# Optimization experiments

Measured on AMD Instinct MI355X. Metric: run time of the kernel, lower is better.

The kernel has to match this reference:

```python
import jax, jax.numpy as jnp
import numpy as np

B, N, D = 64, 1024, 512
H, LD = 8, 64            # num_heads, linear_hidden_dim (H*LD == D)
HIDDEN = 4 * D           # ffn_multiply = 4.0
NB = 128                 # number of timestamp buckets
EPS = 1e-6
TS_SCALE = NB / 14.0     # log1p(1e6) ~ 13.8 -> buckets span [0, NB]


def rms_norm(x, eps=EPS):
    return x * jax.lax.rsqrt(jnp.mean(x * x, axis=-1, keepdims=True) + eps)


def setup_inputs() -> dict:
    key = jax.random.key(0)
    ks = jax.random.split(key, 8)
    lengths = np.linspace(256, N, B).astype(np.int64)
    x_offsets = jnp.asarray(np.concatenate([[0], np.cumsum(lengths)]), dtype=jnp.int64)
    T = int(lengths.sum())
    x = jax.random.normal(ks[0], (T, D), dtype=jnp.float32)
    all_timestamps = jnp.sort(jax.random.randint(ks[1], (B, N), 0, 10**6, dtype=jnp.int64), axis=1)
    invalid_attn_mask = jnp.tril(jnp.ones((N, N), jnp.float32))  # causal
    uv = jax.random.normal(ks[2], (D, 3 * H * LD), dtype=jnp.float32) * 0.02
    pos_w = jax.random.normal(ks[3], (2 * N - 1,), dtype=jnp.float32) * 0.02
    ts_w = jax.random.normal(ks[4], (NB + 1,), dtype=jnp.float32) * 0.02
    w_ams = jax.random.normal(ks[5], (2 * H * LD, D), dtype=jnp.float32) * 0.02
    w1 = jax.random.normal(ks[6], (D, HIDDEN), dtype=jnp.float32) * 0.02
    w2 = jax.random.normal(ks[7], (HIDDEN, D), dtype=jnp.float32) * 0.02
    return {"x": x, "x_offsets": x_offsets, "all_timestamps": all_timestamps,
            "invalid_attn_mask": invalid_attn_mask, "uv": uv, "pos_w": pos_w,
            "ts_w": ts_w, "w_ams": w_ams, "w1": w1, "w2": w2}


def reference(x, x_offsets, all_timestamps, invalid_attn_mask, uv, pos_w, ts_w, w_ams, w1, w2):
    T = x.shape[0]
    # RMSNorm (no learned scale, matches F.rms_norm with no weight) + fused proj + SiLU
    proj = jax.nn.silu(rms_norm(x) @ uv)                       # [T, 3*H*LD]
    u, v = proj[:, :2 * H * LD], proj[:, 2 * H * LD:]          # [T,2HD'], [T,HD']
    # jagged -> padded dense
    tok = jnp.arange(T)
    seg = jnp.searchsorted(x_offsets, tok, side="right") - 1   # batch id per token
    pos = tok - x_offsets[seg]                                  # position within sequence
    padded_v = jnp.zeros((B, N, H * LD), v.dtype).at[seg, pos].set(v).reshape(B, N, H, LD)
    # positional relative bias (batch-independent)
    rel = jnp.arange(N)[:, None] - jnp.arange(N)[None, :]
    pos_attn = pos_w[rel + N - 1] * invalid_attn_mask           # [N,N]
    # temporal relative bias: log-bucketized |t_i - t_j|
    dt = jnp.abs(all_timestamps[:, :, None] - all_timestamps[:, None, :]).astype(jnp.float32)
    bucket = jnp.clip(jnp.floor(jnp.log1p(dt) * TS_SCALE), 0, NB).astype(jnp.int32)
    ts_attn = ts_w[bucket] * invalid_attn_mask[None]            # [B,N,N]
    # two-stream bias 'attention' (no softmax)
    out_pos = jnp.einsum("nm,bmhd->bnhd", pos_attn, padded_v)
    out_ts = jnp.einsum("bnm,bmhd->bnhd", ts_attn, padded_v)
    combined = jnp.concatenate([out_pos, out_ts], axis=-1).reshape(B, N, 2 * H * LD)
    attn_out = combined[seg, pos]                               # dense -> jagged, [T, 2*H*LD]
    # gated norm + multistage FFN with residuals
    ams = u * rms_norm(attn_out)
    h = x + ams @ w_ams
    out = h + jax.nn.silu(rms_norm(h) @ w1) @ w2
    return out
```

## Files before the change

kernel.cpp:

```cpp
#include <hip/hip_runtime.h>
#include <cmath>


using u16 = unsigned short;
using u8  = unsigned char;

typedef __bf16 bf16x8 __attribute__((ext_vector_type(8)));
typedef __bf16 bf16x2 __attribute__((ext_vector_type(2)));
typedef float  f32x4  __attribute__((ext_vector_type(4)));
typedef float  f32x2  __attribute__((ext_vector_type(2)));

#define TS_SCALE_F (float)(128.0 / 14.0)

__device__ __forceinline__ u16 f2b(float f) {
  unsigned u = __float_as_uint(f);
  unsigned r = 0x7FFFu + ((u >> 16) & 1u);
  return (u16)((u + r) >> 16);
}
__device__ __forceinline__ u16 f2b_n(float f) {
  union { __bf16 b; u16 u; } c; c.b = (__bf16)f; return c.u;
}
__device__ __forceinline__ unsigned cvt_pk2(float a, float b) {
  f32x2 v; v[0] = a; v[1] = b;
  bf16x2 r = __builtin_convertvector(v, bf16x2);
  union { bf16x2 b; unsigned u; } c; c.b = r; return c.u;
}
__device__ __forceinline__ float b2f(u16 v) {
  return __uint_as_float(((unsigned)v) << 16);
}
__device__ __forceinline__ bf16x8 as_frag(uint4 r) {
  union { uint4 u; bf16x8 v; } c; c.u = r; return c.v;
}

__device__ __forceinline__ void gload_lds16(const u16* g, u16* l) {
  __builtin_amdgcn_global_load_lds(
      (const __attribute__((address_space(1))) unsigned int*)g,
      (__attribute__((address_space(3))) unsigned int*)l, 16, 0, 0);
}

__device__ __forceinline__ size_t ts_base_u8(int b, int nt) {
  return (size_t)b * 589824 + (size_t)(nt * (nt + 1) / 2) * 16384;
}

__global__ __launch_bounds__(256) void wprep(
    const float* __restrict__ W, u16* __restrict__ Wp, int K, int N)
{
  const int p = blockIdx.x, s = blockIdx.y;
  const int t = threadIdx.x;
  size_t base = ((size_t)p * (K >> 5) + s) * 4096;
  const int e0 = t * 16;
  u16 o[16];
#pragma unroll
  for (int i = 0; i < 16; ++i) {
    int e = e0 + i;
    int kb = e >> 10, r = e & 1023, c = r >> 3, ke = r & 7;
    o[i] = f2b(W[(size_t)(s * 32 + kb * 8 + ke) * N + p * 128 + c]);
  }
  *(uint4*)(Wp + base + e0)     = *(uint4*)o;
  *(uint4*)(Wp + base + e0 + 8) = *(uint4*)(o + 8);
}

#define EPI_SILU_BF16  0
#define EPI_ADD_F32    1
#define EPI_SILU_IMG   2
#define EPI_ADDS       3
#define AM_BF16   0
#define AM_IMG    3
#define AM_BF16M  5

template <int EPI, int AMODE>
__global__ __launch_bounds__(256, 2) void gemm_bf16(
    const u16* __restrict__ A,
    const float* __restrict__ inv, const u16* __restrict__ U, int ustride,
    const u16* __restrict__ Wp, void* __restrict__ C,
    const float* __restrict__ ADD,
    int M, int N, int K, int ncb)
{
  constexpr int NB_ = (AMODE == AM_IMG) ? 2 : 1;
  constexpr int ASZ = (AMODE == AM_IMG) ? 4096 : 5120;
  __shared__ u16 lA[NB_ * ASZ];
  __shared__ u16 lB[NB_ * 4096];

  const int nblk = gridDim.x;
  const int q = nblk >> 3, r = nblk & 7;
  const int xcd = blockIdx.x & 7, li = blockIdx.x >> 3;
  const int work = xcd * q + (xcd < r ? xcd : r) + li;
  const int c0b = work % ncb;
  const int t0  = (work / ncb) * 128;
  const int c0  = c0b * 128;

  const int tid  = threadIdx.x;
  const int wave = tid >> 6, lane = tid & 63;
  const int wr   = (wave >> 1) * 64, wc = (wave & 1) * 64;
  const int l15  = lane & 15, l4 = lane >> 4;

  f32x4 z = {0.f, 0.f, 0.f, 0.f};
  f32x4 acc[4][4];
#pragma unroll
  for (int m = 0; m < 4; ++m)
#pragma unroll
    for (int j = 0; j < 4; ++j) acc[m][j] = z;

  const int ksteps = K >> 5;
  const u16* wsrc = Wp + (size_t)c0b * ksteps * 4096 + wave * 1024 + lane * 8;

  if constexpr (AMODE == AM_IMG) {
    const u16* asrc = A + (size_t)(t0 >> 7) * ksteps * 4096 + wave * 1024 + lane * 8;
    auto stage = [&](int b) {
      u16* sb = &lB[b * 4096 + wave * 1024];
      u16* sa = &lA[b * 4096 + wave * 1024];
      gload_lds16(wsrc,       sb);
      gload_lds16(wsrc + 512, sb + 512);
      gload_lds16(asrc,       sa);
      gload_lds16(asrc + 512, sa + 512);
      wsrc += 4096; asrc += 4096;
    };
    auto compute = [&](int b) {
      bf16x8 afr[4], bfv[4];
#pragma unroll
      for (int m = 0; m < 4; ++m)
        afr[m] = as_frag(*(const uint4*)&lA[b * 4096 + (l4 << 10) + (wr + m * 16 + l15) * 8]);
#pragma unroll
      for (int j = 0; j < 4; ++j)
        bfv[j] = as_frag(*(const uint4*)&lB[b * 4096 + (l4 << 10) + (wc + j * 16 + l15) * 8]);
#pragma unroll
      for (int m = 0; m < 4; ++m)
#pragma unroll
        for (int j = 0; j < 4; ++j)
          acc[m][j] = __builtin_amdgcn_mfma_f32_16x16x32_bf16(afr[m], bfv[j], acc[m][j], 0, 0, 0);
    };
    stage(0);
    int buf = 0;
    for (int s = 0; s + 1 < ksteps; ++s) {
      stage(buf ^ 1);
      asm volatile("s_waitcnt vmcnt(4)" ::: "memory");
      __builtin_amdgcn_s_barrier();
      compute(buf);
      __builtin_amdgcn_s_barrier();
      buf ^= 1;
    }
    asm volatile("s_waitcnt vmcnt(0)" ::: "memory");
    __builtin_amdgcn_s_barrier();
    compute(buf);
  } else {
    const int ar = tid >> 1, ak = (tid & 1) * 16;
    const int row = t0 + ar;
    const bool arow_ok = row < M;
    const u16* ab = A + (size_t)row * K + ak;
    const u16* um = (AMODE == AM_BF16M) ? U + (size_t)row * ustride + ak : nullptr;
    u16* ldsb = &lB[wave * 1024];

    for (int s = 0; s < ksteps; ++s) {
      gload_lds16(wsrc,       ldsb);
      gload_lds16(wsrc + 512, ldsb + 512);
      wsrc += 4096;
      const int k0 = s * 32;
      uint4 pr[4];
      const uint4 z4 = make_uint4(0, 0, 0, 0);
      if (!arow_ok) { pr[0] = z4; pr[1] = z4; pr[2] = z4; pr[3] = z4; }
      else if constexpr (AMODE == AM_BF16) {
        pr[0] = *(const uint4*)(ab + k0);
        pr[1] = *(const uint4*)(ab + k0 + 8);
      } else {
        pr[0] = *(const uint4*)(ab + k0);
        pr[1] = *(const uint4*)(ab + k0 + 8);
        pr[2] = *(const uint4*)(um + k0);
        pr[3] = *(const uint4*)(um + k0 + 8);
      }
      u16 tmp[16];
      unsigned* t32 = (unsigned*)tmp;
      if constexpr (AMODE == AM_BF16) {
        *(uint4*)tmp       = pr[0];
        *(uint4*)(tmp + 8) = pr[1];
      } else {
        const u16* a = (const u16*)pr;
        const u16* u = (const u16*)(pr + 2);
#pragma unroll
        for (int i = 0; i < 8; ++i)
          t32[i] = cvt_pk2(b2f(a[2 * i]) * b2f(u[2 * i]),
                           b2f(a[2 * i + 1]) * b2f(u[2 * i + 1]));
      }
      *(uint4*)&lA[ar * 40 + ak]     = *(uint4*)tmp;
      *(uint4*)&lA[ar * 40 + ak + 8] = *(uint4*)(tmp + 8);
      __syncthreads();

      bf16x8 afr[4], bfv[4];
#pragma unroll
      for (int m = 0; m < 4; ++m)
        afr[m] = as_frag(*(const uint4*)&lA[(wr + m * 16 + l15) * 40 + l4 * 8]);
#pragma unroll
      for (int j = 0; j < 4; ++j)
        bfv[j] = as_frag(*(const uint4*)&lB[(l4 << 10) + (wc + j * 16 + l15) * 8]);
#pragma unroll
      for (int m = 0; m < 4; ++m)
#pragma unroll
        for (int j = 0; j < 4; ++j)
          acc[m][j] = __builtin_amdgcn_mfma_f32_16x16x32_bf16(afr[m], bfv[j], acc[m][j], 0, 0, 0);
      __syncthreads();
    }
  }

#pragma unroll
  for (int m = 0; m < 4; ++m) {
#pragma unroll
    for (int rr = 0; rr < 4; ++rr) {
      int orow = t0 + wr + m * 16 + l4 * 4 + rr;
      if (orow >= M) continue;
      float einv = 0.f;
      if (EPI == EPI_ADDS) einv = inv[orow];
#pragma unroll
      for (int j = 0; j < 4; ++j) {
        int col = c0 + wc + j * 16 + l15;
        float y = acc[m][j][rr];
        if constexpr (EPI == EPI_SILU_BF16) {
          float s = y / (1.f + __expf(-y));
          ((u16*)C)[(size_t)orow * N + col] = f2b_n(s);
        } else if constexpr (EPI == EPI_ADD_F32) {
          size_t idx = (size_t)orow * N + col;
          ((float*)C)[idx] = y + ADD[idx];
        } else if constexpr (EPI == EPI_ADDS) {
          size_t idx = (size_t)orow * N + col;
          ((float*)C)[idx] = y * einv + ADD[idx];
        } else {
          float s = y / (1.f + __expf(-y));
          size_t ioff = ((size_t)(t0 >> 7) * (N >> 5) + (col >> 5)) * 4096
                      + (size_t)((col >> 3) & 3) * 1024
                      + (size_t)(orow & 127) * 8 + (col & 7);
          ((u16*)C)[ioff] = f2b_n(s);
        }
      }
    }
  }
}

__global__ __launch_bounds__(128) void pos_scores(
    const float* __restrict__ pos_w, u16* __restrict__ pos_s)
{
  const int n = blockIdx.x;
  const int m0 = threadIdx.x * 8;
  u16 o[8];
#pragma unroll
  for (int i = 0; i < 8; ++i) {
    int m = m0 + i;
    float v = (m <= n) ? pos_w[n - m + 1023] : 0.f;
    o[i] = f2b(v);
  }
  *(uint4*)(pos_s + (size_t)n * 1024 + m0) = *(uint4*)o;
}

__global__ __launch_bounds__(256) void ts_buckets(
    const int* __restrict__ tstamp, u8* __restrict__ ts_s)
{
  const int nt = 7 - (blockIdx.x >> 6);
  const int b  = blockIdx.x & 63;
  const int W  = 128 * (nt + 1);
  const int n0 = nt * 128;
  const int tid = threadIdx.x;

  __shared__ int tsm[1024];
  for (int i = tid; i < W; i += 256) tsm[i] = tstamp[b * 1024 + i];
  __syncthreads();

  const int r = tid >> 1, h = tid & 1;
  const int n_abs = n0 + r;
  const int t_n = tstamp[b * 1024 + n_abs];
  const int half = W >> 1;
  const int c0 = h * half;
  u8* row = ts_s + ts_base_u8(b, nt) + (size_t)r * W + c0;

  for (int c = 0; c < half; c += 16) {
    u8 o[16];
#pragma unroll
    for (int i = 0; i < 16; ++i) {
      int m = c0 + c + i;
      int d = t_n - tsm[m];
      if (d < 0) d = -d;
      int bkt = (int)(log1pf((float)d) * TS_SCALE_F);
      bkt = bkt > 128 ? 128 : bkt;
      o[i] = (m <= n_abs) ? (u8)bkt : (u8)129;
    }
    *(uint4*)(row + c) = *(uint4*)o;
  }
}

__global__ __launch_bounds__(256, 1) void attn_gemm(
    const u16* __restrict__ proj,
    const int* __restrict__ xoff,
    const u16* __restrict__ pos_s,
    const u8*  __restrict__ tsU8,
    const float* __restrict__ ts_w,
    u16* __restrict__ attn_out,
    int Ttot)
{
  const int flat = blockIdx.x;
  const int nt = 7 - (flat >> 8);
  const int rem = flat & 255;
  const int b  = rem >> 2;
  const int ct = rem & 3;

  const int off = xoff[b];
  int len = xoff[b + 1] - off;
  if (len < 0) len = 0;
  if (len > 1024) len = 1024;
  if (off < 0 || off + len > Ttot) return;
  const int n0 = nt * 128;
  if (n0 >= len) return;
  const int c0 = ct * 128;
  const int W = 128 * (nt + 1);

  __shared__ u16 lP[128 * 40];
  __shared__ u16 lT[128 * 40];
  __shared__ u16 sV[4096];
  __shared__ float s_tsw[130];

  const int tid = threadIdx.x;
  if (tid < 130) s_tsw[tid] = (tid < 129) ? ts_w[tid] : 0.f;
  __syncthreads();

  const int wave = tid >> 6, lane = tid & 63;
  const int wr = (wave >> 1) * 64, wc = (wave & 1) * 64;
  const int l15 = lane & 15, l4 = lane >> 4;

  f32x4 z = {0.f, 0.f, 0.f, 0.f};
  f32x4 accP[4][4], accT[4][4];
#pragma unroll
  for (int m = 0; m < 4; ++m)
#pragma unroll
    for (int j = 0; j < 4; ++j) { accP[m][j] = z; accT[m][j] = z; }

  const int ar = tid >> 1, ak = (tid & 1) * 16;
  const u16* pRow = pos_s + (size_t)(n0 + ar) * 1024 + ak;
  const u8*  tRow = tsU8 + ts_base_u8(b, nt) + (size_t)ar * W + ak;
  const int vk = tid >> 3, vc = (tid & 7) * 16;

  const int mEnd = (n0 + 128 < len) ? (n0 + 128) : len;

  for (int m0 = 0; m0 < mEnd; m0 += 32) {
    {
      int mm = m0 + vk;
      uint4 v0 = make_uint4(0, 0, 0, 0), v1 = v0;
      if (mm < len) {
        const u16* src = proj + (size_t)(off + mm) * 1536 + 1024 + c0 + vc;
        v0 = *(const uint4*)src;
        v1 = *(const uint4*)(src + 8);
      }
      u16 tmp[16];
      *(uint4*)tmp       = v0;
      *(uint4*)(tmp + 8) = v1;
      const int kb = vk >> 3, ke = vk & 7;
#pragma unroll
      for (int i = 0; i < 16; ++i) {
        int col = vc + i;
        int o2 = (kb * 2048 + col * 16 + ke * 2) ^ (((col >> 3) & 7) << 4);
        *(u16*)((char*)sV + o2) = tmp[i];
      }
    }
    {
      uint4 p0 = *(const uint4*)(pRow + m0);
      uint4 p1 = *(const uint4*)(pRow + m0 + 8);
      uint4 tb = *(const uint4*)(tRow + m0);
      const u8* bp = (const u8*)&tb;
      unsigned tt32[8];
#pragma unroll
      for (int i = 0; i < 8; ++i)
        tt32[i] = cvt_pk2(s_tsw[bp[2 * i]], s_tsw[bp[2 * i + 1]]);
      int wb = ar * 40 + ak;
      *(uint4*)&lP[wb]     = p0;
      *(uint4*)&lP[wb + 8] = p1;
      *(uint4*)&lT[wb]     = *(uint4*)tt32;
      *(uint4*)&lT[wb + 8] = *(uint4*)(tt32 + 4);
    }
    __syncthreads();

    bf16x8 ap[4], at[4], bv[4];
#pragma unroll
    for (int m = 0; m < 4; ++m) {
      ap[m] = as_frag(*(const uint4*)&lP[(wr + m * 16 + l15) * 40 + l4 * 8]);
      at[m] = as_frag(*(const uint4*)&lT[(wr + m * 16 + l15) * 40 + l4 * 8]);
    }
#pragma unroll
    for (int j = 0; j < 4; ++j) {
      int col = wc + j * 16 + l15;
      int o2 = (l4 * 2048 + col * 16) ^ (((col >> 3) & 7) << 4);
      bv[j] = as_frag(*(const uint4*)((char*)sV + o2));
    }
#pragma unroll
    for (int m = 0; m < 4; ++m)
#pragma unroll
      for (int j = 0; j < 4; ++j) {
        accP[m][j] = __builtin_amdgcn_mfma_f32_16x16x32_bf16(ap[m], bv[j], accP[m][j], 0, 0, 0);
        accT[m][j] = __builtin_amdgcn_mfma_f32_16x16x32_bf16(at[m], bv[j], accT[m][j], 0, 0, 0);
      }
    __syncthreads();
  }

#pragma unroll
  for (int m = 0; m < 4; ++m)
#pragma unroll
    for (int r = 0; r < 4; ++r) {
      int n = n0 + wr + m * 16 + l4 * 4 + r;
      if (n >= len) continue;
      size_t t = (size_t)(off + n);
#pragma unroll
      for (int j = 0; j < 4; ++j) {
        int hd = c0 + wc + j * 16 + l15;
        int colP = ((hd >> 6) << 7) + (hd & 63);
        attn_out[t * 1024 + colP]      = f2b_n(accP[m][j][r]);
        attn_out[t * 1024 + colP + 64] = f2b_n(accT[m][j][r]);
      }
    }
}

template <int D, bool F32IN, bool WIMG>
__global__ __launch_bounds__(256) void row_ss(
    const void* __restrict__ in, float* __restrict__ inv, u16* __restrict__ aux,
    int T)
{
  const int row = blockIdx.x * 4 + (threadIdx.x >> 6);
  const int lane = threadIdx.x & 63;
  if (row >= T) return;
  float ss = 0.f;
  float v8[8];
  if constexpr (F32IN) {
    const float* r = (const float*)in + (size_t)row * D;
    if constexpr (WIMG) {
      float4 a = *(const float4*)(r + lane * 8);
      float4 b = *(const float4*)(r + lane * 8 + 4);
      v8[0] = a.x; v8[1] = a.y; v8[2] = a.z; v8[3] = a.w;
      v8[4] = b.x; v8[5] = b.y; v8[6] = b.z; v8[7] = b.w;
#pragma unroll
      for (int k = 0; k < 8; ++k) ss += v8[k] * v8[k];
    } else {
#pragma unroll
      for (int i = lane * 4; i < D; i += 256) {
        float4 v = *(const float4*)(r + i);
        ss += v.x * v.x + v.y * v.y + v.z * v.z + v.w * v.w;
      }
    }
  } else {
    const u16* r = (const u16*)in + (size_t)row * D;
#pragma unroll
    for (int i = lane * 8; i < D; i += 512) {
      uint4 v = *(const uint4*)(r + i);
      const u16* q = (const u16*)&v;
#pragma unroll
      for (int k = 0; k < 8; ++k) { float f = b2f(q[k]); ss += f * f; }
    }
  }
#pragma unroll
  for (int o = 32; o > 0; o >>= 1) ss += __shfl_down(ss, o, 64);
  ss = __shfl(ss, 0, 64);
  float rv = rsqrtf(ss / (float)D + 1e-6f);
  if (lane == 0) inv[row] = rv;
  if constexpr (WIMG) {
    unsigned w[4];
#pragma unroll
    for (int i = 0; i < 4; ++i)
      w[i] = cvt_pk2(v8[2 * i] * rv, v8[2 * i + 1] * rv);
    size_t off = (size_t)(row >> 7) * ((D >> 5) * 4096)
               + (size_t)(lane >> 2) * 4096 + (size_t)(lane & 3) * 1024
               + (size_t)(row & 127) * 8;
    *(uint4*)(aux + off) = *(uint4*)w;
  }
}

extern "C" void kernel_launch(void* const* d_in, const int* in_sizes, int n_in,
                              void* d_out, int out_size, void* d_ws, size_t ws_size,
                              hipStream_t stream)
{
  const float* x      = (const float*)d_in[0];
  const int*   xoff   = (const int*)d_in[1];
  const int*   tstamp = (const int*)d_in[2];
  const float* uv     = (const float*)d_in[4];
  const float* pos_w  = (const float*)d_in[5];
  const float* ts_w   = (const float*)d_in[6];
  const float* w_ams  = (const float*)d_in[7];
  const float* w1     = (const float*)d_in[8];
  const float* w2     = (const float*)d_in[9];
  const int T = in_sizes[0] / 512;
  const int nrow = (T + 127) / 128;

  char* ws = (char*)d_ws;
  size_t o = 0;
  auto take = [&](size_t bytes) { size_t r = o; o += (bytes + 255) & ~(size_t)255; return r; };

  u16* uvb    = (u16*)(ws + take((size_t)512 * 1536 * 2));
  u16* wamsb  = (u16*)(ws + take((size_t)1024 * 512 * 2));
  u16* w1b    = (u16*)(ws + take((size_t)512 * 2048 * 2));
  u16* w2b    = (u16*)(ws + take((size_t)2048 * 512 * 2));
  u16* posS   = (u16*)(ws + take((size_t)1024 * 1024 * 2));

  size_t o_ts   = take((size_t)64 * 589824 + 256);
  size_t o_attn = take((size_t)T * 1024 * 2);
  size_t o_proj = take((size_t)T * 1536 * 2 + 131072);
  float* invX = (float*)(ws + take((size_t)T * 4));
  float* invA = (float*)(ws + take((size_t)T * 4));
  float* invH = (float*)(ws + take((size_t)T * 4));

  u8*  tsU8  = (u8*)(ws + o_ts);
  u16* attnS = (u16*)(ws + o_attn);
  u16* proj  = (u16*)(ws + o_proj);
  u16* midI  = (u16*)(ws + o_ts);
  u16* hImg  = (u16*)(ws + o_proj + (size_t)T * 2048);
  u16*   xb  = (u16*)d_out;
  float* h   = (float*)d_out;

  if (ws_size < o) return;

  wprep<<<dim3(12, 16), 256, 0, stream>>>(uv,    uvb,   512,  1536);
  wprep<<<dim3(4, 32),  256, 0, stream>>>(w_ams, wamsb, 1024, 512);
  wprep<<<dim3(16, 16), 256, 0, stream>>>(w1,    w1b,   512,  2048);
  wprep<<<dim3(4, 64),  256, 0, stream>>>(w2,    w2b,   2048, 512);

  pos_scores<<<1024, 128, 0, stream>>>(pos_w, posS);
  ts_buckets<<<512, 256, 0, stream>>>(tstamp, tsU8);

  row_ss<512, true, true><<<(T + 3) / 4, 256, 0, stream>>>(x, invX, xb, T);

  gemm_bf16<EPI_SILU_BF16, AM_IMG><<<12 * nrow, 256, 0, stream>>>(
      xb, nullptr, nullptr, 0, uvb, proj, nullptr, T, 1536, 512, 12);

  attn_gemm<<<64 * 32, 256, 0, stream>>>(proj, xoff, posS, tsU8, ts_w, attnS, T);

  row_ss<1024, false, false><<<(T + 3) / 4, 256, 0, stream>>>(
      attnS, invA, nullptr, T);

  gemm_bf16<EPI_ADDS, AM_BF16M><<<4 * nrow, 256, 0, stream>>>(
      attnS, invA, proj, 1536, wamsb, h, x, T, 512, 1024, 4);

  row_ss<512, true, true><<<(T + 3) / 4, 256, 0, stream>>>(h, invH, hImg, T);

  gemm_bf16<EPI_SILU_IMG, AM_IMG><<<16 * nrow, 256, 0, stream>>>(
      hImg, nullptr, nullptr, 0, w1b, midI, nullptr, T, 2048, 512, 16);

  gemm_bf16<EPI_ADD_F32, AM_IMG><<<4 * nrow, 256, 0, stream>>>(
      midI, nullptr, nullptr, 0, w2b, h, h, T, 512, 2048, 4);
}
```

Measured before the change: 836.7 us.

## Add 256x256-tile 8-wave GEMM with 4-stage LDS pipeline for image-layout GEMMs

Replaces the 128x128 double-buffered GEMM used for the image-layout matmuls (uv projection, w1, w2) with a 512-thread kernel computing 256x256 tiles. It uses a 4-deep LDS ring of 128 KB dynamic shared memory, split half-stages, register prefetch of the next B fragments, and s_setprio around MFMA blocks. The aim is more operand reuse per LDS byte and better overlap of global loads with matrix math. The costs are one block per CU, more padding waste on ragged row counts (the proj buffer slack grows to cover 256-row tiles), and fewer blocks in the grid.

Measured after the change: 1.037 ms. +24.0%, slower.

```diff
diff --git a/kernel.cpp b/kernel.cpp
--- a/kernel.cpp
+++ b/kernel.cpp
@@ -37,6 +37,7 @@
       (const __attribute__((address_space(1))) unsigned int*)g,
       (__attribute__((address_space(3))) unsigned int*)l, 16, 0, 0);
 }
+__device__ __forceinline__ void cfence() { asm volatile("" ::: "memory"); }
 
 __device__ __forceinline__ size_t ts_base_u8(int b, int nt) {
   return (size_t)b * 589824 + (size_t)(nt * (nt + 1) / 2) * 16384;
@@ -64,22 +65,163 @@
 #define EPI_ADD_F32    1
 #define EPI_SILU_IMG   2
 #define EPI_ADDS       3
-#define AM_BF16   0
-#define AM_IMG    3
-#define AM_BF16M  5
-
-template <int EPI, int AMODE>
-__global__ __launch_bounds__(256, 2) void gemm_bf16(
+
+template <int EPI>
+__global__ __launch_bounds__(512, 1) void gemm_img8(
+    const u16* __restrict__ Aimg, const u16* __restrict__ Wp,
+    void* __restrict__ C, const float* __restrict__ ADD,
+    int M, int N, int K, int ncb)
+{
+  extern __shared__ u16 lds[];
+
+  const int nblk = gridDim.x;
+  const int q = nblk >> 3, r = nblk & 7;
+  const int xcd = blockIdx.x & 7, li = blockIdx.x >> 3;
+  const int work = xcd * q + (xcd < r ? xcd : r) + li;
+  const int cb = work % ncb;
+  const int bt = work / ncb;
+  const int t0 = bt * 256, c0 = cb * 256;
+
+  const int tid  = threadIdx.x;
+  const int wave = tid >> 6, lane = tid & 63;
+  const int wm = wave >> 2, wn = wave & 3;
+  const int l15 = lane & 15, l4 = lane >> 4;
+
+  const int nht = K >> 5;
+
+  f32x4 z = {0.f, 0.f, 0.f, 0.f};
+  f32x4 acc[8][4];
+#pragma unroll
+  for (int m = 0; m < 8; ++m)
+#pragma unroll
+    for (int n = 0; n < 4; ++n) acc[m][n] = z;
+
+  const int chunk0 = wave * 4;
+  auto stage2 = [&](int h, int j0) {
+    if (h >= nht) return;
+    u16* hb = &lds[(h & 3) * 16384];
+#pragma unroll
+    for (int j = 0; j < 2; ++j) {
+      int chunk = chunk0 + j0 + j;
+      const u16* src;
+      if (chunk < 16) {
+        int rt = bt * 2 + (chunk >> 3);
+        src = Aimg + ((size_t)rt * nht + h) * 4096 + (size_t)(chunk & 7) * 512
+              + lane * 8;
+      } else {
+        int cp = cb * 2 + ((chunk >> 3) & 1);
+        src = Wp + ((size_t)cp * nht + h) * 4096 + (size_t)(chunk & 7) * 512
+              + lane * 8;
+      }
+      gload_lds16(src, hb + chunk * 512);
+    }
+  };
+
+  bf16x8 aLo[4], aHi[4], bCur[4], bNxt[4];
+  auto readB = [&](int h, bf16x8 (&bf)[4]) {
+    const u16* hb = &lds[(h & 3) * 16384 + 8192];
+#pragma unroll
+    for (int n = 0; n < 4; ++n) {
+      int c = wn * 64 + n * 16 + l15;
+      bf[n] = as_frag(*(const uint4*)&hb[((c >> 7) << 12) + (l4 << 10) + (c & 127) * 8]);
+    }
+  };
+  auto readALo = [&](int h) {
+    const u16* hb = &lds[(h & 3) * 16384];
+#pragma unroll
+    for (int i = 0; i < 4; ++i) {
+      int rw = wm * 128 + i * 16 + l15;
+      aLo[i] = as_frag(*(const uint4*)&hb[((rw >> 7) << 12) + (l4 << 10) + (rw & 127) * 8]);
+    }
+  };
+  auto readAHi = [&](int h) {
+    const u16* hb = &lds[(h & 3) * 16384];
+#pragma unroll
+    for (int i = 0; i < 4; ++i) {
+      int rw = wm * 128 + (4 + i) * 16 + l15;
+      aHi[i] = as_frag(*(const uint4*)&hb[((rw >> 7) << 12) + (l4 << 10) + (rw & 127) * 8]);
+    }
+  };
+
+  stage2(0, 0); stage2(0, 2);
+  stage2(1, 0); stage2(1, 2);
+  stage2(2, 0); stage2(2, 2);
+  asm volatile("s_waitcnt vmcnt(8)" ::: "memory");
+  __builtin_amdgcn_s_barrier();
+  cfence();
+  readALo(0);
+  readB(0, bCur);
+
+  for (int h = 0; h < nht; ++h) {
+    readAHi(h);
+    stage2(h + 3, 0);
+    __builtin_amdgcn_s_barrier();
+    cfence();
+    __builtin_amdgcn_s_setprio(1);
+#pragma unroll
+    for (int i = 0; i < 4; ++i)
+#pragma unroll
+      for (int n = 0; n < 4; ++n)
+        acc[i][n] = __builtin_amdgcn_mfma_f32_16x16x32_bf16(aLo[i], bCur[n], acc[i][n], 0, 0, 0);
+    __builtin_amdgcn_s_setprio(0);
+    __builtin_amdgcn_s_barrier();
+    cfence();
+    stage2(h + 3, 2);
+    asm volatile("s_waitcnt vmcnt(8)" ::: "memory");
+    __builtin_amdgcn_s_barrier();
+    cfence();
+    if (h + 1 < nht) { readALo(h + 1); readB(h + 1, bNxt); }
+    __builtin_amdgcn_s_setprio(1);
+#pragma unroll
+    for (int i = 0; i < 4; ++i)
+#pragma unroll
+      for (int n = 0; n < 4; ++n)
+        acc[4 + i][n] = __builtin_amdgcn_mfma_f32_16x16x32_bf16(aHi[i], bCur[n], acc[4 + i][n], 0, 0, 0);
+    __builtin_amdgcn_s_setprio(0);
+    __builtin_amdgcn_s_barrier();
+    cfence();
+#pragma unroll
+    for (int n = 0; n < 4; ++n) bCur[n] = bNxt[n];
+  }
+
+#pragma unroll
+  for (int m = 0; m < 8; ++m) {
+#pragma unroll
+    for (int rr = 0; rr < 4; ++rr) {
+      int orow = t0 + wm * 128 + m * 16 + l4 * 4 + rr;
+      if (orow >= M) continue;
+#pragma unroll
+      for (int n = 0; n < 4; ++n) {
+        int col = c0 + wn * 64 + n * 16 + l15;
+        float y = acc[m][n][rr];
+        if constexpr (EPI == EPI_SILU_BF16) {
+          float s = y / (1.f + __expf(-y));
+          ((u16*)C)[(size_t)orow * N + col] = f2b_n(s);
+        } else if constexpr (EPI == EPI_ADD_F32) {
+          size_t idx = (size_t)orow * N + col;
+          ((float*)C)[idx] = y + ADD[idx];
+        } else {
+          float s = y / (1.f + __expf(-y));
+          size_t ioff = ((size_t)(orow >> 7) * (N >> 5) + (col >> 5)) * 4096
+                      + (size_t)((col >> 3) & 3) * 1024
+                      + (size_t)(orow & 127) * 8 + (col & 7);
+          ((u16*)C)[ioff] = f2b_n(s);
+        }
+      }
+    }
+  }
+}
+
+template <int EPI>
+__global__ __launch_bounds__(256, 2) void gemm_f(
     const u16* __restrict__ A,
     const float* __restrict__ inv, const u16* __restrict__ U, int ustride,
     const u16* __restrict__ Wp, void* __restrict__ C,
     const float* __restrict__ ADD,
     int M, int N, int K, int ncb)
 {
-  constexpr int NB_ = (AMODE == AM_IMG) ? 2 : 1;
-  constexpr int ASZ = (AMODE == AM_IMG) ? 4096 : 5120;
-  __shared__ u16 lA[NB_ * ASZ];
-  __shared__ u16 lB[NB_ * 4096];
+  __shared__ u16 lA[128 * 40];
+  __shared__ u16 lB[4096];
 
   const int nblk = gridDim.x;
   const int q = nblk >> 3, r = nblk & 7;
@@ -101,103 +243,57 @@
 #pragma unroll
     for (int j = 0; j < 4; ++j) acc[m][j] = z;
 
+  const int ar = tid >> 1, ak = (tid & 1) * 16;
+  const int row = t0 + ar;
+  const bool arow_ok = row < M;
+  const u16* ab = A + (size_t)row * K + ak;
+  const u16* um = U + (size_t)row * ustride + ak;
+
   const int ksteps = K >> 5;
   const u16* wsrc = Wp + (size_t)c0b * ksteps * 4096 + wave * 1024 + lane * 8;
-
-  if constexpr (AMODE == AM_IMG) {
-    const u16* asrc = A + (size_t)(t0 >> 7) * ksteps * 4096 + wave * 1024 + lane * 8;
-    auto stage = [&](int b) {
-      u16* sb = &lB[b * 4096 + wave * 1024];
-      u16* sa = &lA[b * 4096 + wave * 1024];
-      gload_lds16(wsrc,       sb);
-      gload_lds16(wsrc + 512, sb + 512);
-      gload_lds16(asrc,       sa);
-      gload_lds16(asrc + 512, sa + 512);
-      wsrc += 4096; asrc += 4096;
-    };
-    auto compute = [&](int b) {
-      bf16x8 afr[4], bfv[4];
-#pragma unroll
-      for (int m = 0; m < 4; ++m)
-        afr[m] = as_frag(*(const uint4*)&lA[b * 4096 + (l4 << 10) + (wr + m * 16 + l15) * 8]);
+  u16* ldsb = &lB[wave * 1024];
+
+  for (int s = 0; s < ksteps; ++s) {
+    gload_lds16(wsrc,       ldsb);
+    gload_lds16(wsrc + 512, ldsb + 512);
+    wsrc += 4096;
+    const int k0 = s * 32;
+    uint4 pr[4];
+    const uint4 z4 = make_uint4(0, 0, 0, 0);
+    if (!arow_ok) { pr[0] = z4; pr[1] = z4; pr[2] = z4; pr[3] = z4; }
+    else {
+      pr[0] = *(const uint4*)(ab + k0);
+      pr[1] = *(const uint4*)(ab + k0 + 8);
+      pr[2] = *(const uint4*)(um + k0);
+      pr[3] = *(const uint4*)(um + k0 + 8);
+    }
+    u16 tmp[16];
+    unsigned* t32 = (unsigned*)tmp;
+    {
+      const u16* a = (const u16*)pr;
+      const u16* u = (const u16*)(pr + 2);
+#pragma unroll
+      for (int i = 0; i < 8; ++i)
+        t32[i] = cvt_pk2(b2f(a[2 * i]) * b2f(u[2 * i]),
+                         b2f(a[2 * i + 1]) * b2f(u[2 * i + 1]));
+    }
+    *(uint4*)&lA[ar * 40 + ak]     = *(uint4*)tmp;
+    *(uint4*)&lA[ar * 40 + ak + 8] = *(uint4*)(tmp + 8);
+    __syncthreads();
+
+    bf16x8 afr[4], bfv[4];
+#pragma unroll
+    for (int m = 0; m < 4; ++m)
+      afr[m] = as_frag(*(const uint4*)&lA[(wr + m * 16 + l15) * 40 + l4 * 8]);
+#pragma unroll
+    for (int j = 0; j < 4; ++j)
+      bfv[j] = as_frag(*(const uint4*)&lB[(l4 << 10) + (wc + j * 16 + l15) * 8]);
+#pragma unroll
+    for (int m = 0; m < 4; ++m)
 #pragma unroll
       for (int j = 0; j < 4; ++j)
-        bfv[j] = as_frag(*(const uint4*)&lB[b * 4096 + (l4 << 10) + (wc + j * 16 + l15) * 8]);
-#pragma unroll
-      for (int m = 0; m < 4; ++m)
-#pragma unroll
-        for (int j = 0; j < 4; ++j)
-          acc[m][j] = __builtin_amdgcn_mfma_f32_16x16x32_bf16(afr[m], bfv[j], acc[m][j], 0, 0, 0);
-    };
-    stage(0);
-    int buf = 0;
-    for (int s = 0; s + 1 < ksteps; ++s) {
-      stage(buf ^ 1);
-      asm volatile("s_waitcnt vmcnt(4)" ::: "memory");
-      __builtin_amdgcn_s_barrier();
-      compute(buf);
-      __builtin_amdgcn_s_barrier();
-      buf ^= 1;
-    }
-    asm volatile("s_waitcnt vmcnt(0)" ::: "memory");
-    __builtin_amdgcn_s_barrier();
-    compute(buf);
-  } else {
-    const int ar = tid >> 1, ak = (tid & 1) * 16;
-    const int row = t0 + ar;
-    const bool arow_ok = row < M;
-    const u16* ab = A + (size_t)row * K + ak;
-    const u16* um = (AMODE == AM_BF16M) ? U + (size_t)row * ustride + ak : nullptr;
-    u16* ldsb = &lB[wave * 1024];
-
-    for (int s = 0; s < ksteps; ++s) {
-      gload_lds16(wsrc,       ldsb);
-      gload_lds16(wsrc + 512, ldsb + 512);
-      wsrc += 4096;
-      const int k0 = s * 32;
-      uint4 pr[4];
-      const uint4 z4 = make_uint4(0, 0, 0, 0);
-      if (!arow_ok) { pr[0] = z4; pr[1] = z4; pr[2] = z4; pr[3] = z4; }
-      else if constexpr (AMODE == AM_BF16) {
-        pr[0] = *(const uint4*)(ab + k0);
-        pr[1] = *(const uint4*)(ab + k0 + 8);
-      } else {
-        pr[0] = *(const uint4*)(ab + k0);
-        pr[1] = *(const uint4*)(ab + k0 + 8);
-        pr[2] = *(const uint4*)(um + k0);
-        pr[3] = *(const uint4*)(um + k0 + 8);
-      }
-      u16 tmp[16];
-      unsigned* t32 = (unsigned*)tmp;
-      if constexpr (AMODE == AM_BF16) {
-        *(uint4*)tmp       = pr[0];
-        *(uint4*)(tmp + 8) = pr[1];
-      } else {
-        const u16* a = (const u16*)pr;
-        const u16* u = (const u16*)(pr + 2);
-#pragma unroll
-        for (int i = 0; i < 8; ++i)
-          t32[i] = cvt_pk2(b2f(a[2 * i]) * b2f(u[2 * i]),
-                           b2f(a[2 * i + 1]) * b2f(u[2 * i + 1]));
-      }
-      *(uint4*)&lA[ar * 40 + ak]     = *(uint4*)tmp;
-      *(uint4*)&lA[ar * 40 + ak + 8] = *(uint4*)(tmp + 8);
-      __syncthreads();
-
-      bf16x8 afr[4], bfv[4];
-#pragma unroll
-      for (int m = 0; m < 4; ++m)
-        afr[m] = as_frag(*(const uint4*)&lA[(wr + m * 16 + l15) * 40 + l4 * 8]);
-#pragma unroll
-      for (int j = 0; j < 4; ++j)
-        bfv[j] = as_frag(*(const uint4*)&lB[(l4 << 10) + (wc + j * 16 + l15) * 8]);
-#pragma unroll
-      for (int m = 0; m < 4; ++m)
-#pragma unroll
-        for (int j = 0; j < 4; ++j)
-          acc[m][j] = __builtin_amdgcn_mfma_f32_16x16x32_bf16(afr[m], bfv[j], acc[m][j], 0, 0, 0);
-      __syncthreads();
-    }
+        acc[m][j] = __builtin_amdgcn_mfma_f32_16x16x32_bf16(afr[m], bfv[j], acc[m][j], 0, 0, 0);
+    __syncthreads();
   }
 
 #pragma unroll
@@ -206,28 +302,12 @@
     for (int rr = 0; rr < 4; ++rr) {
       int orow = t0 + wr + m * 16 + l4 * 4 + rr;
       if (orow >= M) continue;
-      float einv = 0.f;
-      if (EPI == EPI_ADDS) einv = inv[orow];
+      float einv = inv[orow];
 #pragma unroll
       for (int j = 0; j < 4; ++j) {
         int col = c0 + wc + j * 16 + l15;
-        float y = acc[m][j][rr];
-        if constexpr (EPI == EPI_SILU_BF16) {
-          float s = y / (1.f + __expf(-y));
-          ((u16*)C)[(size_t)orow * N + col] = f2b_n(s);
-        } else if constexpr (EPI == EPI_ADD_F32) {
-          size_t idx = (size_t)orow * N + col;
-          ((float*)C)[idx] = y + ADD[idx];
-        } else if constexpr (EPI == EPI_ADDS) {
-          size_t idx = (size_t)orow * N + col;
-          ((float*)C)[idx] = y * einv + ADD[idx];
-        } else {
-          float s = y / (1.f + __expf(-y));
-          size_t ioff = ((size_t)(t0 >> 7) * (N >> 5) + (col >> 5)) * 4096
-                      + (size_t)((col >> 3) & 3) * 1024
-                      + (size_t)(orow & 127) * 8 + (col & 7);
-          ((u16*)C)[ioff] = f2b_n(s);
-        }
+        size_t idx = (size_t)orow * N + col;
+        ((float*)C)[idx] = acc[m][j][rr] * einv + ADD[idx];
       }
     }
   }
@@ -478,7 +558,8 @@
   const float* w1     = (const float*)d_in[8];
   const float* w2     = (const float*)d_in[9];
   const int T = in_sizes[0] / 512;
-  const int nrow = (T + 127) / 128;
+  const int nrow  = (T + 127) / 128;
+  const int nt256 = (T + 255) / 256;
 
   char* ws = (char*)d_ws;
   size_t o = 0;
@@ -492,7 +573,7 @@
 
   size_t o_ts   = take((size_t)64 * 589824 + 256);
   size_t o_attn = take((size_t)T * 1024 * 2);
-  size_t o_proj = take((size_t)T * 1536 * 2 + 131072);
+  size_t o_proj = take((size_t)T * 1536 * 2 + 786432);
   float* invX = (float*)(ws + take((size_t)T * 4));
   float* invA = (float*)(ws + take((size_t)T * 4));
   float* invH = (float*)(ws + take((size_t)T * 4));
@@ -517,22 +598,22 @@
 
   row_ss<512, true, true><<<(T + 3) / 4, 256, 0, stream>>>(x, invX, xb, T);
 
-  gemm_bf16<EPI_SILU_BF16, AM_IMG><<<12 * nrow, 256, 0, stream>>>(
-      xb, nullptr, nullptr, 0, uvb, proj, nullptr, T, 1536, 512, 12);
+  gemm_img8<EPI_SILU_BF16><<<nt256 * 6, 512, 131072, stream>>>(
+      xb, uvb, proj, nullptr, T, 1536, 512, 6);
 
   attn_gemm<<<64 * 32, 256, 0, stream>>>(proj, xoff, posS, tsU8, ts_w, attnS, T);
 
   row_ss<1024, false, false><<<(T + 3) / 4, 256, 0, stream>>>(
       attnS, invA, nullptr, T);
 
-  gemm_bf16<EPI_ADDS, AM_BF16M><<<4 * nrow, 256, 0, stream>>>(
+  gemm_f<EPI_ADDS><<<4 * nrow, 256, 0, stream>>>(
       attnS, invA, proj, 1536, wamsb, h, x, T, 512, 1024, 4);
 
   row_ss<512, true, true><<<(T + 3) / 4, 256, 0, stream>>>(h, invH, hImg, T);
 
-  gemm_bf16<EPI_SILU_IMG, AM_IMG><<<16 * nrow, 256, 0, stream>>>(
-      hImg, nullptr, nullptr, 0, w1b, midI, nullptr, T, 2048, 512, 16);
-
-  gemm_bf16<EPI_ADD_F32, AM_IMG><<<4 * nrow, 256, 0, stream>>>(
-      midI, nullptr, nullptr, 0, w2b, h, h, T, 512, 2048, 4);
-}
+  gemm_img8<EPI_SILU_IMG><<<nt256 * 8, 512, 131072, stream>>>(
+      hImg, w1b, midI, nullptr, T, 2048, 512, 8);
+
+  gemm_img8<EPI_ADD_F32><<<nt256 * 2, 512, 131072, stream>>>(
+      midI, w2b, h, h, T, 512, 2048, 2);
+}
```

## Deepen AM_IMG GEMM pipeline to four LDS buffers with prefetch distance two

Applied to the files above, without the earlier changes.

The image-layout GEMM path moves from double buffering to a four-slot LDS ring, prefetching two k-steps ahead and dropping the trailing barrier after compute. The aim is to hide more global-load latency and remove one barrier per k-step. The cost is twice the LDS per block for this path, which may reduce occupancy. The four-slot ring is what keeps it safe to skip the second barrier.

New measurement: 901.1 us. 7.7% more time.

```diff
diff --git a/kernel.cpp b/kernel.cpp
--- a/kernel.cpp
+++ b/kernel.cpp
@@ -37,6 +37,7 @@
       (const __attribute__((address_space(1))) unsigned int*)g,
       (__attribute__((address_space(3))) unsigned int*)l, 16, 0, 0);
 }
+__device__ __forceinline__ void cfence() { asm volatile("" ::: "memory"); }
 
 __device__ __forceinline__ size_t ts_base_u8(int b, int nt) {
   return (size_t)b * 589824 + (size_t)(nt * (nt + 1) / 2) * 16384;
@@ -76,7 +77,7 @@
     const float* __restrict__ ADD,
     int M, int N, int K, int ncb)
 {
-  constexpr int NB_ = (AMODE == AM_IMG) ? 2 : 1;
+  constexpr int NB_ = (AMODE == AM_IMG) ? 4 : 1;
   constexpr int ASZ = (AMODE == AM_IMG) ? 4096 : 5120;
   __shared__ u16 lA[NB_ * ASZ];
   __shared__ u16 lB[NB_ * 4096];
@@ -102,20 +103,24 @@
     for (int j = 0; j < 4; ++j) acc[m][j] = z;
 
   const int ksteps = K >> 5;
-  const u16* wsrc = Wp + (size_t)c0b * ksteps * 4096 + wave * 1024 + lane * 8;
+  const u16* wsrc0 = Wp + (size_t)c0b * ksteps * 4096 + wave * 1024 + lane * 8;
 
   if constexpr (AMODE == AM_IMG) {
-    const u16* asrc = A + (size_t)(t0 >> 7) * ksteps * 4096 + wave * 1024 + lane * 8;
-    auto stage = [&](int b) {
+    const u16* asrc0 = A + (size_t)(t0 >> 7) * ksteps * 4096 + wave * 1024 + lane * 8;
+    auto stage = [&](int s) {
+      if (s >= ksteps) return;
+      const int b = s & 3;
       u16* sb = &lB[b * 4096 + wave * 1024];
       u16* sa = &lA[b * 4096 + wave * 1024];
-      gload_lds16(wsrc,       sb);
-      gload_lds16(wsrc + 512, sb + 512);
-      gload_lds16(asrc,       sa);
-      gload_lds16(asrc + 512, sa + 512);
-      wsrc += 4096; asrc += 4096;
+      const u16* ws = wsrc0 + (size_t)s * 4096;
+      const u16* as = asrc0 + (size_t)s * 4096;
+      gload_lds16(ws,       sb);
+      gload_lds16(ws + 512, sb + 512);
+      gload_lds16(as,       sa);
+      gload_lds16(as + 512, sa + 512);
     };
-    auto compute = [&](int b) {
+    auto compute = [&](int s) {
+      const int b = s & 3;
       bf16x8 afr[4], bfv[4];
 #pragma unroll
       for (int m = 0; m < 4; ++m)
@@ -130,18 +135,16 @@
           acc[m][j] = __builtin_amdgcn_mfma_f32_16x16x32_bf16(afr[m], bfv[j], acc[m][j], 0, 0, 0);
     };
     stage(0);
-    int buf = 0;
-    for (int s = 0; s + 1 < ksteps; ++s) {
-      stage(buf ^ 1);
-      asm volatile("s_waitcnt vmcnt(4)" ::: "memory");
+    stage(1);
+    for (int s = 0; s < ksteps; ++s) {
+      stage(s + 2);
+      if (s + 2 < ksteps)      asm volatile("s_waitcnt vmcnt(8)" ::: "memory");
+      else if (s + 1 < ksteps) asm volatile("s_waitcnt vmcnt(4)" ::: "memory");
+      else                     asm volatile("s_waitcnt vmcnt(0)" ::: "memory");
       __builtin_amdgcn_s_barrier();
-      compute(buf);
-      __builtin_amdgcn_s_barrier();
-      buf ^= 1;
-    }
-    asm volatile("s_waitcnt vmcnt(0)" ::: "memory");
-    __builtin_amdgcn_s_barrier();
-    compute(buf);
+      cfence();
+      compute(s);
+    }
   } else {
     const int ar = tid >> 1, ak = (tid & 1) * 16;
     const int row = t0 + ar;
@@ -149,6 +152,7 @@
     const u16* ab = A + (size_t)row * K + ak;
     const u16* um = (AMODE == AM_BF16M) ? U + (size_t)row * ustride + ak : nullptr;
     u16* ldsb = &lB[wave * 1024];
+    const u16* wsrc = wsrc0;
 
     for (int s = 0; s < ksteps; ++s) {
       gload_lds16(wsrc,       ldsb);
```
